# Optimization experiments

Measured on AMD Instinct MI355X. Metric: run time of the kernel, lower is better.

## Reference

```python
import jax, jax.numpy as jnp
import numpy as np

B, N, D = 16, 1024, 768
H = 12
HD = D // H
HID = 4 * D
EPS = 1e-6


def _layernorm(x, g, b):
    mu = jnp.mean(x, axis=-1, keepdims=True)
    var = jnp.mean(jnp.square(x - mu), axis=-1, keepdims=True)
    return (x - mu) * jax.lax.rsqrt(var + EPS) * g + b


def setup_inputs() -> dict:
    key = jax.random.key(0)
    ks = jax.random.split(key, 8)
    s_d = 1.0 / np.sqrt(D)
    s_h = 1.0 / np.sqrt(HID)
    return {
        "x": jax.random.normal(ks[0], (B, N, D), dtype=jnp.float32),
        "qkv_w": jax.random.uniform(ks[1], (3 * D, D), jnp.float32, -s_d, s_d),
        "proj_w": jax.random.uniform(ks[2], (D, D), jnp.float32, -s_d, s_d),
        "proj_b": jax.random.uniform(ks[3], (D,), jnp.float32, -s_d, s_d),
        "fc1_w": jax.random.uniform(ks[4], (HID, D), jnp.float32, -s_d, s_d),
        "fc1_b": jax.random.uniform(ks[5], (HID,), jnp.float32, -s_d, s_d),
        "fc2_w": jax.random.uniform(ks[6], (D, HID), jnp.float32, -s_h, s_h),
        "fc2_b": jax.random.uniform(ks[7], (D,), jnp.float32, -s_h, s_h),
        "norm1_g": jnp.ones((D,), jnp.float32),
        "norm1_b": jnp.zeros((D,), jnp.float32),
        "norm2_g": jnp.ones((D,), jnp.float32),
        "norm2_b": jnp.zeros((D,), jnp.float32),
    }


def _attention(x, qkv_w, proj_w, proj_b):
    b, n, _ = x.shape
    qkv = x @ qkv_w.T                                  # [b,n,3D] (no bias: qkv_bias=False)
    qkv = qkv.reshape(b, n, 3, H, HD)
    q, k, v = (jnp.transpose(qkv[:, :, i], (0, 2, 1, 3)) for i in range(3))  # [b,h,n,hd]
    scale = HD ** (-0.5)
    dots = jnp.einsum("bhid,bhjd->bhij", q, k) * scale
    attn = jax.nn.softmax(dots, axis=-1)
    out = jnp.einsum("bhij,bhjd->bhid", attn, v)
    out = jnp.transpose(out, (0, 2, 1, 3)).reshape(b, n, H * HD)
    return out @ proj_w.T + proj_b


def _mlp(x, fc1_w, fc1_b, fc2_w, fc2_b):
    h = jax.nn.gelu(x @ fc1_w.T + fc1_b, approximate=False)
    return h @ fc2_w.T + fc2_b


def reference(x, qkv_w, proj_w, proj_b, fc1_w, fc1_b, fc2_w, fc2_b,
              norm1_g, norm1_b, norm2_g, norm2_b):
    x = x + _attention(_layernorm(x, norm1_g, norm1_b), qkv_w, proj_w, proj_b)
    x = x + _mlp(_layernorm(x, norm2_g, norm2_b), fc1_w, fc1_b, fc2_w, fc2_b)
    return x
```

## Files before the change

### kernel.cpp

```cpp
#include <hip/hip_runtime.h>
#include <hip/hip_bf16.h>
#include <math.h>

using bf16 = __hip_bfloat16;
typedef __attribute__((ext_vector_type(8))) short short8;
typedef __attribute__((ext_vector_type(4))) short shortx4;
typedef __attribute__((ext_vector_type(4))) float floatx4;

#define BB 16
#define NN 1024
#define DD 768
#define HH 12
#define HD 64
#define HID 3072

__device__ __forceinline__ floatx4 mfma_bf16(short8 a, short8 b, floatx4 c) {
  return __builtin_amdgcn_mfma_f32_16x16x32_bf16(a, b, c, 0, 0, 0);
}

__device__ __forceinline__ short bf16_bits(float f) {
  union { bf16 h; short s; } u;
  u.h = __float2bfloat16(f);
  return u.s;
}

__device__ __forceinline__ void async_copy16(const void* g, void* l) {
  __builtin_amdgcn_global_load_lds(
      (const __attribute__((address_space(1))) unsigned int*)g,
      (__attribute__((address_space(3))) unsigned int*)l,
      16, 0, 0);
}

__device__ __forceinline__ float gelu_f(float x) {
  const float z = x * fmaf(0.10294324f, x * x, 2.3022082f);
  const float e = exp2f(z);
  return x - x * __builtin_amdgcn_rcpf(e + 1.0f);
}

__global__ __launch_bounds__(256)
void cvt_kernel(const float* __restrict__ in, bf16* __restrict__ out, int n4)
{
  const int i = blockIdx.x * 256 + threadIdx.x;
  if (i >= n4) return;
  const float4 v = ((const float4*)in)[i];
  shortx4 o;
  o.x = bf16_bits(v.x); o.y = bf16_bits(v.y);
  o.z = bf16_bits(v.z); o.w = bf16_bits(v.w);
  ((shortx4*)out)[i] = o;
}

__global__ __launch_bounds__(256)
void ln_kernel(const float* __restrict__ x, const float* __restrict__ g,
               const float* __restrict__ b, bf16* __restrict__ y)
{
  const int row = blockIdx.x;
  const int t = threadIdx.x;
  const float* xr = x + (size_t)row * DD;
  float v[3];
  float s = 0.f, s2 = 0.f;
#pragma unroll
  for (int i = 0; i < 3; ++i) {
    float f = xr[t + i * 256];
    v[i] = f;
    s += f;
    s2 += f * f;
  }
#pragma unroll
  for (int off = 1; off < 64; off <<= 1) {
    s  += __shfl_xor(s, off);
    s2 += __shfl_xor(s2, off);
  }
  __shared__ float red[2][4];
  const int wave = t >> 6, lane = t & 63;
  if (lane == 0) { red[0][wave] = s; red[1][wave] = s2; }
  __syncthreads();
  s  = red[0][0] + red[0][1] + red[0][2] + red[0][3];
  s2 = red[1][0] + red[1][1] + red[1][2] + red[1][3];
  const float mu = s * (1.f / DD);
  const float var = s2 * (1.f / DD) - mu * mu;
  const float inv = rsqrtf(var + 1e-6f);
  bf16* yr = y + (size_t)row * DD;
#pragma unroll
  for (int i = 0; i < 3; ++i) {
    int c = t + i * 256;
    yr[c] = __float2bfloat16((v[i] - mu) * inv * g[c] + b[c]);
  }
}

template <int EPI>
__global__ __launch_bounds__(512, 2)
void gemm_kernel(const bf16* __restrict__ A, const bf16* __restrict__ W,
                 const float* __restrict__ bias, const float* __restrict__ res,
                 void* __restrict__ Cv, int N, int K)
{
  __shared__ __align__(16) short smem[65536];

  const int tid  = threadIdx.x;
  const int lane = tid & 63;
  const int w    = tid >> 6;
  const int wm   = w >> 2;
  const int wn   = w & 3;
  const int row16 = lane & 15, quad = lane >> 4;

  const int gx = gridDim.x, gy = gridDim.y;
  const int lin = blockIdx.y * gx + blockIdx.x;
  const int PP  = (gy & 7) ? gy : 8;
  const int per = gx * PP;
  const int pan = lin / per, rem = lin % per;
  const int bm = (pan * PP + rem % PP) * 256;
  const int bn = (rem / PP) * 256;

  const int rloc = lane >> 2;
  const int cl   = lane & 3;
  const int swzs = (rloc & 3) ^ ((rloc >> 2) & 3);
  const int cg   = cl ^ swzs;
  const bf16* Ag = A + (size_t)(bm + w * 32 + rloc) * K + cg * 8;
  const bf16* Bg = W + (size_t)(bn + w * 32 + rloc) * K + cg * 8;
  const size_t a16 = (size_t)16 * K;
  const int stLds = w * 1024;

  const int NS = K >> 5;

  const int swzr = (row16 & 3) ^ ((row16 >> 2) & 3);
  const int cx   = (quad ^ swzr) * 8;

#define SLOT(u) (((u) & 3) * 16384)
#define STAGE_A(u, ko) do { \
    async_copy16(Ag + (ko),        smem + SLOT(u) + stLds); \
    async_copy16(Ag + a16 + (ko),  smem + SLOT(u) + stLds + 512); } while (0)
#define STAGE_B(u, ko) do { \
    async_copy16(Bg + (ko),        smem + SLOT(u) + 8192 + stLds); \
    async_copy16(Bg + a16 + (ko),  smem + SLOT(u) + 8192 + stLds + 512); } while (0)

  for (int u = 0; u < 3; ++u) {
    const size_t ko = (size_t)u * 32;
    STAGE_A(u, ko);
    STAGE_B(u, ko);
  }

  floatx4 acc[8][4] = {};

  asm volatile("s_waitcnt vmcnt(8)" ::: "memory");
  __builtin_amdgcn_s_barrier();

  for (int s = 0; s < NS; ++s) {
    int u = s + 3; if (u >= NS) u -= NS;
    const size_t ko = (size_t)u * 32;
    const short* sAs = smem + SLOT(s);
    const short* sBs = sAs + 8192;

    short8 af[4], bfr[4];
#pragma unroll
    for (int mt = 0; mt < 4; ++mt)
      af[mt] = *(const short8*)&sAs[(wm * 128 + mt * 16 + row16) * 32 + cx];
#pragma unroll
    for (int nt = 0; nt < 4; ++nt)
      bfr[nt] = *(const short8*)&sBs[(wn * 64 + nt * 16 + row16) * 32 + cx];
    STAGE_A(u, ko);
    __builtin_amdgcn_s_barrier();
    __builtin_amdgcn_s_setprio(1);
#pragma unroll
    for (int mt = 0; mt < 4; ++mt)
#pragma unroll
      for (int nt = 0; nt < 4; ++nt)
        acc[mt][nt] = mfma_bf16(bfr[nt], af[mt], acc[mt][nt]);
    __builtin_amdgcn_s_setprio(0);
    __builtin_amdgcn_s_barrier();

    short8 af2[4];
#pragma unroll
    for (int mt = 0; mt < 4; ++mt)
      af2[mt] = *(const short8*)&sAs[(wm * 128 + (mt + 4) * 16 + row16) * 32 + cx];
    STAGE_B(u, ko);
    __builtin_amdgcn_s_barrier();
    __builtin_amdgcn_s_setprio(1);
#pragma unroll
    for (int mt = 0; mt < 4; ++mt)
#pragma unroll
      for (int nt = 0; nt < 4; ++nt)
        acc[mt + 4][nt] = mfma_bf16(bfr[nt], af2[mt], acc[mt + 4][nt]);
    __builtin_amdgcn_s_setprio(0);
    asm volatile("s_waitcnt vmcnt(8)" ::: "memory");
    __builtin_amdgcn_s_barrier();
  }
  asm volatile("s_waitcnt vmcnt(0)" ::: "memory");
#undef SLOT
#undef STAGE_A
#undef STAGE_B

  floatx4 bias4[4] = {};
  if (EPI != 0) {
#pragma unroll
    for (int nt = 0; nt < 4; ++nt)
      bias4[nt] = *(const floatx4*)&bias[bn + wn * 64 + nt * 16 + quad * 4];
  }

#pragma unroll
  for (int mt = 0; mt < 8; ++mt) {
    const int row = bm + wm * 128 + mt * 16 + row16;
    if (EPI == 1) {
      const float* rr = res + (size_t)row * N;
      float* cr = (float*)Cv + (size_t)row * N;
#pragma unroll
      for (int nt = 0; nt < 4; ++nt) {
        const int col = bn + wn * 64 + nt * 16 + quad * 4;
        const floatx4 rv = *(const floatx4*)&rr[col];
        floatx4 o;
#pragma unroll
        for (int r = 0; r < 4; ++r) o[r] = acc[mt][nt][r] + bias4[nt][r] + rv[r];
        *(floatx4*)&cr[col] = o;
      }
    } else {
      bf16* cr = (bf16*)Cv + (size_t)row * N;
#pragma unroll
      for (int nt = 0; nt < 4; ++nt) {
        const int col = bn + wn * 64 + nt * 16 + quad * 4;
        shortx4 pk;
#pragma unroll
        for (int r = 0; r < 4; ++r) {
          float v = acc[mt][nt][r] + bias4[nt][r];
          if (EPI == 2) v = gelu_f(v);
          pk[r] = bf16_bits(v);
        }
        *(shortx4*)&cr[col] = pk;
      }
    }
  }
}

__global__ __launch_bounds__(256)
void vtrans_kernel(const bf16* __restrict__ qkv, bf16* __restrict__ vt)
{
  const int bh = blockIdx.y;
  const int b = bh / HH, h = bh % HH;
  const int n0 = blockIdx.x * 64;
  __shared__ __align__(16) short tile[64 * 72];
  const int tid = threadIdx.x;

  const int r = tid >> 2, c16 = (tid & 3) * 16;
  const bf16* src = qkv + (size_t)(b * NN + n0 + r) * 2304 + 2 * DD + h * 64 + c16;
  *(short8*)&tile[r * 72 + c16]     = *(const short8*)(src);
  *(short8*)&tile[r * 72 + c16 + 8] = *(const short8*)(src + 8);
  __syncthreads();

#pragma unroll
  for (int it = 0; it < 2; ++it) {
    const int d  = (tid >> 3) + it * 32;
    const int jg = (tid & 7) * 8;
    short8 o;
#pragma unroll
    for (int t = 0; t < 8; ++t) ((short*)&o)[t] = tile[(jg + t) * 72 + d];
    *(short8*)&vt[((size_t)bh * 64 + d) * NN + n0 + jg] = o;
  }
}

__global__ __launch_bounds__(256, 2)
void attn_kernel(const bf16* __restrict__ qkv, const bf16* __restrict__ vt,
                 bf16* __restrict__ out)
{
  const int bh = blockIdx.y;
  const int b = bh / HH, h = bh % HH;
  const int q0 = blockIdx.x * 128;
  const int tid = threadIdx.x;
  const int lane = tid & 63;
  const int wave = tid >> 6;
  const int row16 = lane & 15, quad = lane >> 4;

  __shared__ __align__(16) short sK[64 * 72];
  __shared__ __align__(16) short sVt[64 * 72];
  __shared__ __align__(16) short sP[4][32 * 72];

  const bf16* base  = qkv + (size_t)b * NN * 2304 + h * 64;
  const bf16* vbase = vt + (size_t)bh * 64 * NN;

  short8 qf[2][2];
#pragma unroll
  for (int qg = 0; qg < 2; ++qg) {
    const bf16* qrow = base + (size_t)(q0 + wave * 32 + qg * 16 + row16) * 2304;
    qf[qg][0] = *(const short8*)(qrow + quad * 8);
    qf[qg][1] = *(const short8*)(qrow + 32 + quad * 8);
  }

  floatx4 o_acc[2][4] = {};
  floatx4 l_acc[2] = {};
  const short8 ones = { (short)0x3F80, (short)0x3F80, (short)0x3F80, (short)0x3F80,
                        (short)0x3F80, (short)0x3F80, (short)0x3F80, (short)0x3F80 };

  const int sr = tid >> 2;
  const int sc = (tid & 3) * 16;
  const float ESC = 0.1803368801f;

  for (int jt = 0; jt < NN / 64; ++jt) {
    const int j0 = jt * 64;
    {
      const bf16* kp = base + (size_t)(j0 + sr) * 2304 + DD + sc;
      *(short8*)&sK[sr * 72 + sc]     = *(const short8*)(kp);
      *(short8*)&sK[sr * 72 + sc + 8] = *(const short8*)(kp + 8);
      const bf16* vp = vbase + (size_t)sr * NN + j0 + sc;
      *(short8*)&sVt[sr * 72 + sc]     = *(const short8*)(vp);
      *(short8*)&sVt[sr * 72 + sc + 8] = *(const short8*)(vp + 8);
    }
    __syncthreads();

#pragma unroll
    for (int nt = 0; nt < 4; ++nt) {
      short8 kb0 = *(const short8*)&sK[(nt * 16 + row16) * 72 + quad * 8];
      short8 kb1 = *(const short8*)&sK[(nt * 16 + row16) * 72 + 32 + quad * 8];
#pragma unroll
      for (int qg = 0; qg < 2; ++qg) {
        floatx4 st = {};
        st = mfma_bf16(kb0, qf[qg][0], st);
        st = mfma_bf16(kb1, qf[qg][1], st);
        shortx4 pk;
#pragma unroll
        for (int r = 0; r < 4; ++r)
          pk[r] = bf16_bits(exp2f(fminf(st[r] * ESC, 30.f)));
        *(shortx4*)&sP[wave][(qg * 16 + row16) * 72 + nt * 16 + quad * 4] = pk;
      }
    }

    short8 vb[4][2];
#pragma unroll
    for (int dt = 0; dt < 4; ++dt) {
      vb[dt][0] = *(const short8*)&sVt[(dt * 16 + row16) * 72 + quad * 8];
      vb[dt][1] = *(const short8*)&sVt[(dt * 16 + row16) * 72 + 32 + quad * 8];
    }
#pragma unroll
    for (int qg = 0; qg < 2; ++qg) {
      short8 pf0 = *(const short8*)&sP[wave][(qg * 16 + row16) * 72 + quad * 8];
      short8 pf1 = *(const short8*)&sP[wave][(qg * 16 + row16) * 72 + 32 + quad * 8];
      l_acc[qg] = mfma_bf16(pf0, ones, l_acc[qg]);
      l_acc[qg] = mfma_bf16(pf1, ones, l_acc[qg]);
#pragma unroll
      for (int dt = 0; dt < 4; ++dt) {
        o_acc[qg][dt] = mfma_bf16(pf0, vb[dt][0], o_acc[qg][dt]);
        o_acc[qg][dt] = mfma_bf16(pf1, vb[dt][1], o_acc[qg][dt]);
      }
    }
    __syncthreads();
  }

#pragma unroll
  for (int qg = 0; qg < 2; ++qg) {
#pragma unroll
    for (int r = 0; r < 4; ++r) {
      const float inv = 1.f / l_acc[qg][r];
      const size_t n = (size_t)(b * NN + q0 + wave * 32 + qg * 16 + quad * 4 + r);
#pragma unroll
      for (int dt = 0; dt < 4; ++dt) {
        out[n * DD + h * 64 + dt * 16 + row16] =
            __float2bfloat16(o_acc[qg][dt][r] * inv);
      }
    }
  }
}

extern "C" void kernel_launch(void* const* d_in, const int* in_sizes, int n_in,
                              void* d_out, int out_size, void* d_ws, size_t ws_size,
                              hipStream_t stream)
{
  const float* x       = (const float*)d_in[0];
  const float* qkv_w   = (const float*)d_in[1];
  const float* proj_w  = (const float*)d_in[2];
  const float* proj_b  = (const float*)d_in[3];
  const float* fc1_w   = (const float*)d_in[4];
  const float* fc1_b   = (const float*)d_in[5];
  const float* fc2_w   = (const float*)d_in[6];
  const float* fc2_b   = (const float*)d_in[7];
  const float* norm1_g = (const float*)d_in[8];
  const float* norm1_b = (const float*)d_in[9];
  const float* norm2_g = (const float*)d_in[10];
  const float* norm2_b = (const float*)d_in[11];
  float* out = (float*)d_out;

  const int M = BB * NN;
  char* ws = (char*)d_ws;

  bf16* wq = (bf16*)ws;
  bf16* wp = wq + (size_t)3 * DD * DD;
  bf16* w1 = wp + (size_t)DD * DD;
  bf16* w2 = w1 + (size_t)HID * DD;
  bf16* xn = w2 + (size_t)DD * HID;
  char* p2 = (char*)(xn + (size_t)M * DD);
  const size_t base_b = (size_t)(p2 - ws);

  int NBc = 1;
  for (int c = 16; c >= 1; c >>= 1)
    if (ws_size >= base_b + (size_t)c * 1024 * 7680) { NBc = c; break; }

  const int Rc = NBc * NN;
  bf16* qkvb = (bf16*)p2;
  bf16* aob  = qkvb + (size_t)Rc * 2304;
  bf16* vtb  = aob  + (size_t)Rc * DD;
  bf16* hb   = (bf16*)p2;

  cvt_kernel<<<(3 * DD * DD / 4 + 255) / 256, 256, 0, stream>>>(qkv_w, wq, 3 * DD * DD / 4);
  cvt_kernel<<<(DD * DD / 4 + 255) / 256, 256, 0, stream>>>(proj_w, wp, DD * DD / 4);
  cvt_kernel<<<(HID * DD / 4 + 255) / 256, 256, 0, stream>>>(fc1_w, w1, HID * DD / 4);
  cvt_kernel<<<(DD * HID / 4 + 255) / 256, 256, 0, stream>>>(fc2_w, w2, DD * HID / 4);

  ln_kernel<<<M, 256, 0, stream>>>(x, norm1_g, norm1_b, xn);

  for (int c = 0; c < BB / NBc; ++c) {
    const size_t r0 = (size_t)c * Rc;
    gemm_kernel<0><<<dim3(3 * DD / 256, Rc / 256), 512, 0, stream>>>(
        xn + r0 * DD, wq, nullptr, nullptr, qkvb, 3 * DD, DD);
    vtrans_kernel<<<dim3(NN / 64, NBc * HH), 256, 0, stream>>>(qkvb, vtb);
    attn_kernel<<<dim3(NN / 128, NBc * HH), 256, 0, stream>>>(qkvb, vtb, aob);
    gemm_kernel<1><<<dim3(DD / 256, Rc / 256), 512, 0, stream>>>(
        aob, wp, proj_b, x + r0 * DD, out + r0 * DD, DD, DD);
  }

  ln_kernel<<<M, 256, 0, stream>>>(out, norm2_g, norm2_b, xn);

  for (int c = 0; c < BB / NBc; ++c) {
    const size_t r0 = (size_t)c * Rc;
    gemm_kernel<2><<<dim3(HID / 256, Rc / 256), 512, 0, stream>>>(
        xn + r0 * DD, w1, fc1_b, nullptr, hb, HID, DD);
    gemm_kernel<1><<<dim3(DD / 256, Rc / 256), 512, 0, stream>>>(
        hb, w2, fc2_b, out + r0 * DD, out + r0 * DD, DD, HID);
  }
}
```

Before: 596.7 us.

## Template GEMM on tile size, use 128-tiles for N=768 GEMMs with double buffering

```diff
diff --git a/kernel.cpp b/kernel.cpp
--- a/kernel.cpp
+++ b/kernel.cpp
@@ -87,13 +87,21 @@
   }
 }
 
-template <int EPI>
-__global__ __launch_bounds__(512, 2)
+template <int EPI, int TF>
+__global__ __launch_bounds__(512, (TF == 16) ? 4 : 6)
 void gemm_kernel(const bf16* __restrict__ A, const bf16* __restrict__ W,
                  const float* __restrict__ bias, const float* __restrict__ res,
                  void* __restrict__ Cv, int N, int K)
 {
-  __shared__ __align__(16) short smem[65536];
+  constexpr int BM   = TF * 16;
+  constexpr int MF   = TF / 2;
+  constexpr int NF   = TF / 4;
+  constexpr int ACA  = TF / 8;
+  constexpr int ACB  = TF / 8;
+  constexpr int ASZ  = TF * 512;
+  constexpr int SLT  = 2 * ASZ;
+
+  __shared__ __align__(16) short smem[2 * SLT];
 
   const int tid  = threadIdx.x;
   const int lane = tid & 63;
@@ -107,103 +115,85 @@
   const int PP  = (gy & 7) ? gy : 8;
   const int per = gx * PP;
   const int pan = lin / per, rem = lin % per;
-  const int bm = (pan * PP + rem % PP) * 256;
-  const int bn = (rem / PP) * 256;
-
-  const int rloc = lane >> 2;
-  const int cl   = lane & 3;
-  const int swzs = (rloc & 3) ^ ((rloc >> 2) & 3);
-  const int cg   = cl ^ swzs;
-  const bf16* Ag = A + (size_t)(bm + w * 32 + rloc) * K + cg * 8;
-  const bf16* Bg = W + (size_t)(bn + w * 32 + rloc) * K + cg * 8;
-  const size_t a16 = (size_t)16 * K;
-  const int stLds = w * 1024;
+  const int bm = (pan * PP + rem % PP) * BM;
+  const int bn = (rem / PP) * BM;
+
+  const int rl = lane & 15;
+  const int kl = lane >> 4;
+  const bf16* Asrc = A + (size_t)(bm + w * (16 * ACA) + rl) * K + kl * 8;
+  const bf16* Bsrc = W + (size_t)(bn + w * (16 * ACB) + rl) * K + kl * 8;
 
   const int NS = K >> 5;
 
-  const int swzr = (row16 & 3) ^ ((row16 >> 2) & 3);
-  const int cx   = (quad ^ swzr) * 8;
-
-#define SLOT(u) (((u) & 3) * 16384)
-#define STAGE_A(u, ko) do { \
-    async_copy16(Ag + (ko),        smem + SLOT(u) + stLds); \
-    async_copy16(Ag + a16 + (ko),  smem + SLOT(u) + stLds + 512); } while (0)
-#define STAGE_B(u, ko) do { \
-    async_copy16(Bg + (ko),        smem + SLOT(u) + 8192 + stLds); \
-    async_copy16(Bg + a16 + (ko),  smem + SLOT(u) + 8192 + stLds + 512); } while (0)
-
-  for (int u = 0; u < 3; ++u) {
-    const size_t ko = (size_t)u * 32;
-    STAGE_A(u, ko);
-    STAGE_B(u, ko);
-  }
-
-  floatx4 acc[8][4] = {};
-
-  asm volatile("s_waitcnt vmcnt(8)" ::: "memory");
-  __builtin_amdgcn_s_barrier();
+  auto STAGE_A = [&](int slot, int ko) {
+    short* d = smem + slot * SLT + w * (ACA * 512);
+#pragma unroll
+    for (int c = 0; c < ACA; ++c)
+      async_copy16(Asrc + (size_t)c * 16 * K + ko, d + c * 512);
+  };
+  auto STAGE_B = [&](int slot, int ko) {
+    short* d = smem + slot * SLT + ASZ + w * (ACB * 512);
+#pragma unroll
+    for (int c = 0; c < ACB; ++c)
+      async_copy16(Bsrc + (size_t)c * 16 * K + ko, d + c * 512);
+  };
+
+  STAGE_A(0, 0);
+  STAGE_B(0, 0);
+
+  floatx4 acc[MF][NF] = {};
 
   for (int s = 0; s < NS; ++s) {
-    int u = s + 3; if (u >= NS) u -= NS;
-    const size_t ko = (size_t)u * 32;
-    const short* sAs = smem + SLOT(s);
-    const short* sBs = sAs + 8192;
-
-    short8 af[4], bfr[4];
-#pragma unroll
-    for (int mt = 0; mt < 4; ++mt)
-      af[mt] = *(const short8*)&sAs[(wm * 128 + mt * 16 + row16) * 32 + cx];
-#pragma unroll
-    for (int nt = 0; nt < 4; ++nt)
-      bfr[nt] = *(const short8*)&sBs[(wn * 64 + nt * 16 + row16) * 32 + cx];
-    STAGE_A(u, ko);
+    const int cur = s & 1, nxt = cur ^ 1;
+    const short* slot = smem + cur * SLT;
+    const bool pf = (s + 1 < NS);
+
+    if (pf) {
+      STAGE_A(nxt, (s + 1) * 32);
+      if constexpr (ACA == 2)
+        asm volatile("s_waitcnt vmcnt(2)" ::: "memory");
+      else
+        asm volatile("s_waitcnt vmcnt(1)" ::: "memory");
+    } else {
+      asm volatile("s_waitcnt vmcnt(0)" ::: "memory");
+    }
     __builtin_amdgcn_s_barrier();
+
+    short8 bfr[NF];
+#pragma unroll
+    for (int nt = 0; nt < NF; ++nt)
+      bfr[nt] = *(const short8*)&slot[ASZ + (wn * NF + nt) * 512 + lane * 8];
+
+    if (pf) STAGE_B(nxt, (s + 1) * 32);
+
     __builtin_amdgcn_s_setprio(1);
 #pragma unroll
-    for (int mt = 0; mt < 4; ++mt)
-#pragma unroll
-      for (int nt = 0; nt < 4; ++nt)
-        acc[mt][nt] = mfma_bf16(bfr[nt], af[mt], acc[mt][nt]);
+    for (int mt = 0; mt < MF; ++mt) {
+      const short8 af = *(const short8*)&slot[(wm * MF + mt) * 512 + lane * 8];
+#pragma unroll
+      for (int nt = 0; nt < NF; ++nt)
+        acc[mt][nt] = mfma_bf16(bfr[nt], af, acc[mt][nt]);
+    }
     __builtin_amdgcn_s_setprio(0);
     __builtin_amdgcn_s_barrier();
-
-    short8 af2[4];
-#pragma unroll
-    for (int mt = 0; mt < 4; ++mt)
-      af2[mt] = *(const short8*)&sAs[(wm * 128 + (mt + 4) * 16 + row16) * 32 + cx];
-    STAGE_B(u, ko);
-    __builtin_amdgcn_s_barrier();
-    __builtin_amdgcn_s_setprio(1);
-#pragma unroll
-    for (int mt = 0; mt < 4; ++mt)
-#pragma unroll
-      for (int nt = 0; nt < 4; ++nt)
-        acc[mt + 4][nt] = mfma_bf16(bfr[nt], af2[mt], acc[mt + 4][nt]);
-    __builtin_amdgcn_s_setprio(0);
-    asm volatile("s_waitcnt vmcnt(8)" ::: "memory");
-    __builtin_amdgcn_s_barrier();
-  }
-  asm volatile("s_waitcnt vmcnt(0)" ::: "memory");
-#undef SLOT
-#undef STAGE_A
-#undef STAGE_B
-
-  floatx4 bias4[4] = {};
+  }
+
+  floatx4 bias4[NF] = {};
   if (EPI != 0) {
 #pragma unroll
-    for (int nt = 0; nt < 4; ++nt)
-      bias4[nt] = *(const floatx4*)&bias[bn + wn * 64 + nt * 16 + quad * 4];
-  }
-
-#pragma unroll
-  for (int mt = 0; mt < 8; ++mt) {
-    const int row = bm + wm * 128 + mt * 16 + row16;
+    for (int nt = 0; nt < NF; ++nt)
+      bias4[nt] = *(const floatx4*)&bias[bn + wn * (NF * 16) + nt * 16 + quad * 4];
+  }
+
+#pragma unroll
+  for (int mt = 0; mt < MF; ++mt) {
+    const int row = bm + wm * (MF * 16) + mt * 16 + row16;
     if (EPI == 1) {
       const float* rr = res + (size_t)row * N;
       float* cr = (float*)Cv + (size_t)row * N;
 #pragma unroll
-      for (int nt = 0; nt < 4; ++nt) {
-        const int col = bn + wn * 64 + nt * 16 + quad * 4;
+      for (int nt = 0; nt < NF; ++nt) {
+        const int col = bn + wn * (NF * 16) + nt * 16 + quad * 4;
         const floatx4 rv = *(const floatx4*)&rr[col];
         floatx4 o;
 #pragma unroll
@@ -213,8 +203,8 @@
     } else {
       bf16* cr = (bf16*)Cv + (size_t)row * N;
 #pragma unroll
-      for (int nt = 0; nt < 4; ++nt) {
-        const int col = bn + wn * 64 + nt * 16 + quad * 4;
+      for (int nt = 0; nt < NF; ++nt) {
+        const int col = bn + wn * (NF * 16) + nt * 16 + quad * 4;
         shortx4 pk;
 #pragma unroll
         for (int r = 0; r < 4; ++r) {
@@ -403,11 +393,11 @@
 
   for (int c = 0; c < BB / NBc; ++c) {
     const size_t r0 = (size_t)c * Rc;
-    gemm_kernel<0><<<dim3(3 * DD / 256, Rc / 256), 512, 0, stream>>>(
+    gemm_kernel<0, 16><<<dim3(3 * DD / 256, Rc / 256), 512, 0, stream>>>(
         xn + r0 * DD, wq, nullptr, nullptr, qkvb, 3 * DD, DD);
     vtrans_kernel<<<dim3(NN / 64, NBc * HH), 256, 0, stream>>>(qkvb, vtb);
     attn_kernel<<<dim3(NN / 128, NBc * HH), 256, 0, stream>>>(qkvb, vtb, aob);
-    gemm_kernel<1><<<dim3(DD / 256, Rc / 256), 512, 0, stream>>>(
+    gemm_kernel<1, 8><<<dim3(DD / 128, Rc / 128), 512, 0, stream>>>(
         aob, wp, proj_b, x + r0 * DD, out + r0 * DD, DD, DD);
   }
 
@@ -415,9 +405,9 @@
 
   for (int c = 0; c < BB / NBc; ++c) {
     const size_t r0 = (size_t)c * Rc;
-    gemm_kernel<2><<<dim3(HID / 256, Rc / 256), 512, 0, stream>>>(
+    gemm_kernel<2, 16><<<dim3(HID / 256, Rc / 256), 512, 0, stream>>>(
         xn + r0 * DD, w1, fc1_b, nullptr, hb, HID, DD);
-    gemm_kernel<1><<<dim3(DD / 256, Rc / 256), 512, 0, stream>>>(
+    gemm_kernel<1, 8><<<dim3(DD / 128, Rc / 128), 512, 0, stream>>>(
         hb, w2, fc2_b, out + r0 * DD, out + r0 * DD, DD, HID);
   }
 }
```

After: 1.592 ms. +166.9%, slower.
